# Performance work log

Measured on AMD Instinct MI355X. Metric: run time of the kernel, lower is better.

Reference implementation:

```python
import jax, jax.numpy as jnp
import numpy as np

NODES = 512
SCALE_S, SCALE_M, SCALE_L = 512, 1024, 2048
BATCH = 16
SEQ = SCALE_S + SCALE_M + SCALE_L
EPS = 1e-5


def setup_inputs() -> dict:
    key = jax.random.key(0)
    ks = jax.random.split(key, 10)
    sd = 1.0 / np.sqrt(NODES)
    inp = {
        "x": jax.random.normal(ks[0], (BATCH, SEQ, NODES), dtype=jnp.float32),
        "gamma": jnp.ones((NODES,), jnp.float32),
        "beta": jnp.zeros((NODES,), jnp.float32),
        "Wqkv_s": jax.random.normal(ks[1], (NODES, 3 * NODES), jnp.float32) * sd,
        "bqkv_s": jnp.zeros((3 * NODES,), jnp.float32),
        "Wqkv_m": jax.random.normal(ks[2], (NODES, 3 * NODES), jnp.float32) * sd,
        "bqkv_m": jnp.zeros((3 * NODES,), jnp.float32),
        "Wqkv_l": jax.random.normal(ks[3], (NODES, 3 * NODES), jnp.float32) * sd,
        "bqkv_l": jnp.zeros((3 * NODES,), jnp.float32),
        "Wout": jax.random.normal(ks[4], (NODES, NODES), jnp.float32) * sd,
        "bout": jnp.zeros((NODES,), jnp.float32),
    }
    return inp


def _attn_block(x, W, b, scaling):
    # x: [B, L, N]; fused QKV projection then single-head attention
    qkv = jnp.einsum("bln,nm->blm", x, W) + b
    q, k, v = jnp.split(qkv, 3, axis=-1)
    scores = jnp.einsum("bqn,bkn->bqk", q, k) * scaling
    attn = jax.nn.softmax(scores, axis=-1)
    return jnp.einsum("bqk,bkn->bqn", attn, v)


def reference(x, gamma, beta, Wqkv_s, bqkv_s, Wqkv_m, bqkv_m, Wqkv_l, bqkv_l, Wout, bout):
    res = x
    mu = jnp.mean(x, axis=-1, keepdims=True)
    var = jnp.mean(jnp.square(x - mu), axis=-1, keepdims=True)
    h = (x - mu) * jax.lax.rsqrt(var + EPS) * gamma + beta

    scaling = NODES ** (-0.5)
    xs = h[:, :SCALE_S, :]
    xm = h[:, SCALE_S:SCALE_S + SCALE_M, :]
    xl = h[:, SCALE_S + SCALE_M:SCALE_S + SCALE_M + SCALE_L, :]

    out_s = _attn_block(xs, Wqkv_s, bqkv_s, scaling)
    out_m = _attn_block(xm, Wqkv_m, bqkv_m, scaling)
    out_l = _attn_block(xl, Wqkv_l, bqkv_l, scaling)

    out = jnp.concatenate([out_s, out_m, out_l], axis=1)
    out = jnp.einsum("bln,nm->blm", out, Wout) + bout
    return out + res
```

## Files before the change

kernel.cpp:

```cpp
#include <hip/hip_runtime.h>
#include <stdint.h>

typedef __bf16 bf16;
typedef __bf16 bf16x8 __attribute__((ext_vector_type(8)));
typedef __bf16 bf16x4 __attribute__((ext_vector_type(4)));
typedef float f32x4 __attribute__((ext_vector_type(4)));

#define MFMA16(a, b, c) __builtin_amdgcn_mfma_f32_16x16x32_bf16(a, b, c, 0, 0, 0)

typedef const __attribute__((address_space(1))) uint32_t* gas_t;
typedef __attribute__((address_space(3))) uint32_t* las_t;

__device__ __forceinline__ void gload16(const void* g, void* l) {
  __builtin_amdgcn_global_load_lds((gas_t)g, (las_t)l, 16, 0, 0);
}

__device__ __forceinline__ void stage_tile(const bf16* __restrict__ A, int lda,
                                           const bf16* __restrict__ Bt, int ldb,
                                           int m0, int n0, int k0, bf16* Ad,
                                           bf16* Bd, int w, int r8, int cs) {
#pragma unroll
  for (int i = 0; i < 4; ++i) {
    const int ii = (w << 2) + i;
    const int row = (ii << 3) + r8;
    gload16(A + (size_t)(m0 + row) * lda + k0 + (cs << 3), Ad + (ii << 9));
    gload16(Bt + (size_t)(n0 + row) * ldb + k0 + (cs << 3), Bd + (ii << 9));
  }
}

__device__ __forceinline__ void compute_tile(const bf16* As, const bf16* Bs,
                                             f32x4 (*acc)[4], int lane, int wm,
                                             int wn) {
#pragma unroll
  for (int kk = 0; kk < 2; ++kk) {
    bf16x8 af[4], bfr[4];
#pragma unroll
    for (int mi = 0; mi < 4; ++mi) {
      const int r = wm * 64 + mi * 16 + (lane & 15);
      const int ch = kk * 4 + (lane >> 4);
      af[mi] = *(const bf16x8*)((const char*)As + r * 128 + ((ch ^ (r & 7)) << 4));
    }
#pragma unroll
    for (int ni = 0; ni < 4; ++ni) {
      const int r = wn * 64 + ni * 16 + (lane & 15);
      const int ch = kk * 4 + (lane >> 4);
      bfr[ni] = *(const bf16x8*)((const char*)Bs + r * 128 + ((ch ^ (r & 7)) << 4));
    }
#pragma unroll
    for (int mi = 0; mi < 4; ++mi)
#pragma unroll
      for (int ni = 0; ni < 4; ++ni)
        acc[mi][ni] = MFMA16(af[mi], bfr[ni], acc[mi][ni]);
  }
}

__device__ __forceinline__ void gemm_core(const bf16* __restrict__ A, int lda,
                                          const bf16* __restrict__ Bt, int ldb,
                                          int nk, int m0, int n0,
                                          bf16 (*smem)[128 * 64],
                                          f32x4 (*acc)[4]) {
  const int t = threadIdx.x;
  const int lane = t & 63, w = t >> 6;
  const int wm = w >> 1, wn = w & 1;
  const int r8 = lane >> 3;
  const int cs = (lane & 7) ^ r8;

  stage_tile(A, lda, Bt, ldb, m0, n0, 0, smem[0], smem[2], w, r8, cs);
  __syncthreads();
  int cur = 0;
  for (int kt = 0; kt < nk; ++kt) {
    if (kt + 1 < nk)
      stage_tile(A, lda, Bt, ldb, m0, n0, (kt + 1) << 6, smem[cur ^ 1],
                 smem[2 + (cur ^ 1)], w, r8, cs);
    compute_tile(smem[cur], smem[2 + cur], acc, lane, wm, wn);
    __syncthreads();
    cur ^= 1;
  }
}

__device__ __forceinline__ void epi_put(float* lds, const f32x4* accmi,
                                        int lane, int wm, int wn) {
#pragma unroll
  for (int ni = 0; ni < 4; ++ni) {
    const int c = wn * 64 + ni * 16 + (lane & 15);
    const int lr0 = wm * 16 + ((lane >> 4) << 2);
#pragma unroll
    for (int r = 0; r < 4; ++r) {
      const int lr = lr0 + r;
      lds[(lr << 7) + ((((c >> 2) ^ (lr & 7)) << 2) | (c & 3))] = accmi[ni][r];
    }
  }
}

__device__ __forceinline__ void epi_get(const float* lds, int t, f32x4* v) {
  const int lr = t >> 3, ch0 = (t & 7) << 2;
#pragma unroll
  for (int j = 0; j < 4; ++j)
    v[j] = *(const f32x4*)(lds + (lr << 7) + (((ch0 + j) ^ (lr & 7)) << 2));
}

__global__ __launch_bounds__(256) void transpose_all(
    const float* __restrict__ Ws, const float* __restrict__ Wm,
    const float* __restrict__ Wl, const float* __restrict__ Wo,
    bf16* __restrict__ os, bf16* __restrict__ om, bf16* __restrict__ ol,
    bf16* __restrict__ oo) {
  __shared__ float tile[32][33];
  const int id = blockIdx.x;
  const float* in;
  bf16* outp;
  int N, bx;
  if (id < 768) { in = Ws; outp = os; N = 1536; bx = id; }
  else if (id < 1536) { in = Wm; outp = om; N = 1536; bx = id - 768; }
  else if (id < 2304) { in = Wl; outp = ol; N = 1536; bx = id - 1536; }
  else { in = Wo; outp = oo; N = 512; bx = id - 2304; }
  const int nbx = N >> 5;
  const int n0 = (bx % nbx) * 32, k0 = (bx / nbx) * 32;
  const int tx = threadIdx.x, ty = threadIdx.y;
#pragma unroll
  for (int i = 0; i < 4; ++i)
    tile[ty * 4 + i][tx] = in[(size_t)(k0 + ty * 4 + i) * N + n0 + tx];
  __syncthreads();
#pragma unroll
  for (int i = 0; i < 4; ++i)
    outp[(size_t)(n0 + ty * 4 + i) * 512 + k0 + tx] = (bf16)tile[tx][ty * 4 + i];
}

__global__ __launch_bounds__(256) void conv_v(const float* __restrict__ Ws,
                                              const float* __restrict__ Wm,
                                              const float* __restrict__ Wl,
                                              bf16* __restrict__ Bs,
                                              bf16* __restrict__ Bm,
                                              bf16* __restrict__ Bl) {
  int id = blockIdx.x;
  const float* W;
  bf16* B;
  if (id < 256) { W = Ws; B = Bs; }
  else if (id < 512) { W = Wm; B = Bm; id -= 256; }
  else { W = Wl; B = Bl; id -= 512; }
  const int idx = (id * 256 + threadIdx.x) * 4;
  const int k = idx >> 9, j = idx & 511;
  float4 v = *(const float4*)(W + (size_t)k * 1536 + 1024 + j);
  bf16x4 o = {(bf16)v.x, (bf16)v.y, (bf16)v.z, (bf16)v.w};
  *(bf16x4*)(B + idx) = o;
}

__global__ __launch_bounds__(256) void wprep(const bf16* __restrict__ wto,
                                             const bf16* __restrict__ Bs,
                                             const bf16* __restrict__ Bm,
                                             const bf16* __restrict__ Bl,
                                             bf16* __restrict__ ws_,
                                             bf16* __restrict__ wm_,
                                             bf16* __restrict__ wl_) {
  __shared__ bf16 smem[4][128 * 64];
  const int t = threadIdx.x, lane = t & 63, w = t >> 6;
  const int wm = w >> 1, wn = w & 1;
  const int id = blockIdx.x;
  const int sc = id >> 4, rem = id & 15;
  const bf16* Bv;
  bf16* dst;
  if (sc == 0) { Bv = Bs; dst = ws_; }
  else if (sc == 1) { Bv = Bm; dst = wm_; }
  else { Bv = Bl; dst = wl_; }
  dst += 1024 * 512;
  const int m0 = (rem >> 2) << 7, n0 = (rem & 3) << 7;

  f32x4 acc[4][4];
#pragma unroll
  for (int i = 0; i < 4; ++i)
#pragma unroll
    for (int j = 0; j < 4; ++j) acc[i][j] = (f32x4)0.0f;

  gemm_core(wto, 512, Bv, 512, 8, m0, n0, smem, acc);

  float* et = (float*)smem;
#pragma unroll
  for (int mi = 0; mi < 4; ++mi) epi_put(et + (mi << 12), acc[mi], lane, wm, wn);
  __syncthreads();
  const int lr = t >> 3, c0l = (t & 7) << 4;
#pragma unroll
  for (int mi = 0; mi < 4; ++mi) {
    f32x4 v[4];
    epi_get(et + (mi << 12), t, v);
    const int grow = m0 + ((lr >> 4) << 6) + mi * 16 + (lr & 15);
    bf16x8 o0, o1;
#pragma unroll
    for (int j = 0; j < 4; ++j)
#pragma unroll
      for (int k = 0; k < 4; ++k) {
        const bf16 val = (bf16)v[j][k];
        if (j < 2) o0[j * 4 + k] = val;
        else o1[(j - 2) * 4 + k] = val;
      }
    bf16* d = dst + (size_t)grow * 512 + n0 + c0l;
    *(bf16x8*)d = o0;
    *(bf16x8*)(d + 8) = o1;
  }
}

__global__ __launch_bounds__(512) void bias_prep(const float* __restrict__ bs,
                                                 const float* __restrict__ bm,
                                                 const float* __restrict__ bl,
                                                 const float* __restrict__ Wout,
                                                 float* __restrict__ ps,
                                                 float* __restrict__ pm,
                                                 float* __restrict__ pl) {
  const float* b;
  float* p;
  if (blockIdx.x == 0) { b = bs; p = ps; }
  else if (blockIdx.x == 1) { b = bm; p = pm; }
  else { b = bl; p = pl; }
  const int t = threadIdx.x;
  p[t] = b[t];
  p[512 + t] = b[512 + t];
  float acc = 0.0f;
  for (int n = 0; n < 512; ++n) acc += b[1024 + n] * Wout[(size_t)n * 512 + t];
  p[1024 + t] = acc;
}

__global__ __launch_bounds__(256) void ln_kernel(const float* __restrict__ x,
                                                 const float* __restrict__ gamma,
                                                 const float* __restrict__ beta,
                                                 bf16* __restrict__ h) {
  const int t = threadIdx.x, lane = t & 63, w = t >> 6;
  const int row = blockIdx.x * 4 + w;
  const float* xr = x + (size_t)row * 512 + lane * 8;
  float4 v0 = *(const float4*)xr;
  float4 v1 = *(const float4*)(xr + 4);
  float s = v0.x + v0.y + v0.z + v0.w + v1.x + v1.y + v1.z + v1.w;
  float q = v0.x * v0.x + v0.y * v0.y + v0.z * v0.z + v0.w * v0.w +
            v1.x * v1.x + v1.y * v1.y + v1.z * v1.z + v1.w * v1.w;
#pragma unroll
  for (int off = 1; off < 64; off <<= 1) {
    s += __shfl_xor(s, off);
    q += __shfl_xor(q, off);
  }
  const float mean = s * (1.0f / 512.0f);
  const float var = q * (1.0f / 512.0f) - mean * mean;
  const float rs = rsqrtf(var + 1e-5f);
  float4 g0 = *(const float4*)(gamma + lane * 8);
  float4 g1 = *(const float4*)(gamma + lane * 8 + 4);
  float4 b0 = *(const float4*)(beta + lane * 8);
  float4 b1 = *(const float4*)(beta + lane * 8 + 4);
  const int bb = row / 3584;
  const int sp = row - bb * 3584;
  size_t drow;
  if (sp < 512)
    drow = (size_t)bb * 512 + sp;
  else if (sp < 1536)
    drow = 8192 + (size_t)bb * 1024 + (sp - 512);
  else
    drow = 24576 + (size_t)bb * 2048 + (sp - 1536);
  bf16x8 ov = {(bf16)((v0.x - mean) * rs * g0.x + b0.x),
               (bf16)((v0.y - mean) * rs * g0.y + b0.y),
               (bf16)((v0.z - mean) * rs * g0.z + b0.z),
               (bf16)((v0.w - mean) * rs * g0.w + b0.w),
               (bf16)((v1.x - mean) * rs * g1.x + b1.x),
               (bf16)((v1.y - mean) * rs * g1.y + b1.y),
               (bf16)((v1.z - mean) * rs * g1.z + b1.z),
               (bf16)((v1.w - mean) * rs * g1.w + b1.w)};
  *(bf16x8*)(h + drow * 512 + lane * 8) = ov;
}

__device__ __forceinline__ void qkv_body(const bf16* __restrict__ A,
                                         const bf16* __restrict__ Bt,
                                         const float* __restrict__ bias,
                                         bf16* __restrict__ qk,
                                         bf16* __restrict__ vt, int l2L,
                                         int lgs, bf16 (*smem)[128 * 64]) {
  const int t = threadIdx.x, lane = t & 63, w = t >> 6;
  const int wm = w >> 1, wn = w & 1;
  const int m0 = (lgs / 12) << 7;
  const int n0 = (lgs % 12) << 7;
  const int L = 1 << l2L;

  f32x4 acc[4][4];
#pragma unroll
  for (int i = 0; i < 4; ++i)
#pragma unroll
    for (int j = 0; j < 4; ++j) acc[i][j] = (f32x4)0.0f;

  gemm_core(A, 512, Bt, 512, 8, m0, n0, smem, acc);

  if (n0 < 1024) {
    float* et = (float*)smem;
#pragma unroll
    for (int mi = 0; mi < 4; ++mi) epi_put(et + (mi << 12), acc[mi], lane, wm, wn);
    __syncthreads();
    const int lr = t >> 3, c0l = (t & 7) << 4;
    const int gcol = n0 + c0l;
#pragma unroll
    for (int mi = 0; mi < 4; ++mi) {
      f32x4 v[4];
      epi_get(et + (mi << 12), t, v);
      const int grow = m0 + ((lr >> 4) << 6) + mi * 16 + (lr & 15);
      bf16x8 o0, o1;
#pragma unroll
      for (int j = 0; j < 4; ++j) {
        float4 bv = *(const float4*)(bias + gcol + j * 4);
#pragma unroll
        for (int k = 0; k < 4; ++k) {
          const bf16 val = (bf16)(v[j][k] + ((const float*)&bv)[k]);
          if (j < 2) o0[j * 4 + k] = val;
          else o1[(j - 2) * 4 + k] = val;
        }
      }
      bf16* dst = qk + (size_t)grow * 1024 + gcol;
      *(bf16x8*)dst = o0;
      *(bf16x8*)(dst + 8) = o1;
    }
  } else {
#pragma unroll
    for (int ni = 0; ni < 4; ++ni) {
      const int col = n0 + wn * 64 + ni * 16 + (lane & 15);
      const float bv = bias[col];
#pragma unroll
      for (int mi = 0; mi < 4; ++mi) {
        const int rb = m0 + wm * 64 + mi * 16 + ((lane >> 4) << 2);
        const int d = col - 1024;
        const int bi = rb >> l2L;
        const int kv = rb & (L - 1);
        bf16x4 pk = {(bf16)(acc[mi][ni][0] + bv), (bf16)(acc[mi][ni][1] + bv),
                     (bf16)(acc[mi][ni][2] + bv), (bf16)(acc[mi][ni][3] + bv)};
        *(bf16x4*)(vt + ((size_t)bi * 512 + d) * L + kv) = pk;
      }
    }
  }
}

__global__ __launch_bounds__(256) void qkv_all(
    const bf16* __restrict__ h, const bf16* __restrict__ wt_s,
    const bf16* __restrict__ wt_m, const bf16* __restrict__ wt_l,
    const float* __restrict__ pb_s, const float* __restrict__ pb_m,
    const float* __restrict__ pb_l, bf16* __restrict__ qk,
    bf16* __restrict__ vt) {
  __shared__ bf16 smem[4][128 * 64];
  const int lg = (blockIdx.x & 7) * (5376 >> 3) + (blockIdx.x >> 3);
  if (lg < 768) {
    qkv_body(h, wt_s, pb_s, qk, vt, 9, lg, smem);
  } else if (lg < 2304) {
    qkv_body(h + 8192ull * 512, wt_m, pb_m, qk + 8192ull * 1024,
             vt + 4194304ull, 10, lg - 768, smem);
  } else {
    qkv_body(h + 24576ull * 512, wt_l, pb_l, qk + 24576ull * 1024,
             vt + 12582912ull, 11, lg - 2304, smem);
  }
}

__global__ __launch_bounds__(256) void sgemm_one(const bf16* __restrict__ qkp,
                                                 bf16* __restrict__ Cb, int l2L,
                                                 int b0, float scl2, int nblk,
                                                 float* __restrict__ psum) {
  __shared__ bf16 smem[4][128 * 64];
  const int t = threadIdx.x, lane = t & 63, w = t >> 6;
  const int wm = w >> 1, wn = w & 1;
  const int L = 1 << l2L;
  const int l2nt = l2L - 7;
  const int lgs = (blockIdx.x & 7) * (nblk >> 3) + (blockIdx.x >> 3);
  const int bi = lgs >> (2 * l2nt);
  const int rem = lgs & ((1 << (2 * l2nt)) - 1);
  const int m0 = (rem >> l2nt) << 7;
  const int n0 = (rem & ((1 << l2nt) - 1)) << 7;

  const bf16* Ab = qkp + (size_t)(b0 + bi) * L * 1024;
  const bf16* Bb = Ab + 512;
  bf16* C = Cb + (size_t)bi * L * L;

  f32x4 acc[4][4];
#pragma unroll
  for (int i = 0; i < 4; ++i)
#pragma unroll
    for (int j = 0; j < 4; ++j) acc[i][j] = (f32x4)0.0f;

  gemm_core(Ab, 1024, Bb, 1024, 8, m0, n0, smem, acc);

  float* et = (float*)smem;
#pragma unroll
  for (int mi = 0; mi < 4; ++mi) epi_put(et + (mi << 12), acc[mi], lane, wm, wn);
  __syncthreads();
  const int lr = t >> 3, c0l = (t & 7) << 4;
  const int tilej = n0 >> 7;
#pragma unroll
  for (int mi = 0; mi < 4; ++mi) {
    f32x4 v[4];
    epi_get(et + (mi << 12), t, v);
    const int grow = m0 + ((lr >> 4) << 6) + mi * 16 + (lr & 15);
    bf16x8 o0, o1;
    float ps = 0.0f;
#pragma unroll
    for (int j = 0; j < 4; ++j)
#pragma unroll
      for (int k = 0; k < 4; ++k) {
        const float e = exp2f(v[j][k] * scl2);
        const bf16 val = (bf16)e;
        ps += (float)val;
        if (j < 2) o0[j * 4 + k] = val;
        else o1[(j - 2) * 4 + k] = val;
      }
    bf16* dst = C + (size_t)grow * L + n0 + c0l;
    *(bf16x8*)dst = o0;
    *(bf16x8*)(dst + 8) = o1;
    ps += __shfl_xor(ps, 1);
    ps += __shfl_xor(ps, 2);
    ps += __shfl_xor(ps, 4);
    if ((t & 7) == 0) psum[((size_t)(bi * L + grow) << 4) + tilej] = ps;
  }
}

__global__ __launch_bounds__(256) void pv_one(const bf16* __restrict__ sb,
                                              const bf16* __restrict__ vtp,
                                              float* __restrict__ out,
                                              const float* __restrict__ x,
                                              const float* __restrict__ bout,
                                              int l2L, int b0, int seqoff,
                                              int nblk,
                                              const float* __restrict__ psum) {
  __shared__ bf16 smem[4][128 * 64];
  const int t = threadIdx.x, lane = t & 63, w = t >> 6;
  const int wm = w >> 1, wn = w & 1;
  const int L = 1 << l2L;
  const int l2nt = l2L - 7;
  const int ntile = 1 << l2nt;
  const int lgs = (blockIdx.x & 7) * (nblk >> 3) + (blockIdx.x >> 3);
  const int bi = lgs >> (l2nt + 2);
  const int rem = lgs & ((1 << (l2nt + 2)) - 1);
  const int m0 = (rem >> 2) << 7;
  const int n0 = (rem & 3) << 7;
  const int b = b0 + bi;

  const bf16* Ab = sb + (size_t)bi * L * L;
  const bf16* Bb = vtp + (size_t)b * 512 * L;

  f32x4 acc[4][4];
#pragma unroll
  for (int i = 0; i < 4; ++i)
#pragma unroll
    for (int j = 0; j < 4; ++j) acc[i][j] = (f32x4)0.0f;

  gemm_core(Ab, L, Bb, L, L >> 6, m0, n0, smem, acc);

  float* et = (float*)smem;
#pragma unroll
  for (int mi = 0; mi < 4; ++mi) epi_put(et + (mi << 12), acc[mi], lane, wm, wn);
  __syncthreads();
  const int lr = t >> 3, c0l = (t & 7) << 4;
  const int gcol = n0 + c0l;
  float4 bvv[4];
#pragma unroll
  for (int j = 0; j < 4; ++j) bvv[j] = *(const float4*)(bout + gcol + j * 4);
#pragma unroll
  for (int mi = 0; mi < 4; ++mi) {
    f32x4 v[4];
    epi_get(et + (mi << 12), t, v);
    const int grow = m0 + ((lr >> 4) << 6) + mi * 16 + (lr & 15);
    const float* pr = psum + ((size_t)(bi * L + grow) << 4);
    float rs = 0.0f;
    for (int j = 0; j < ntile; ++j) rs += pr[j];
    const float inv = 1.0f / rs;
    const size_t g = (size_t)b * 3584 + seqoff + grow;
    const float* xs = x + g * 512 + gcol;
    float* os = out + g * 512 + gcol;
#pragma unroll
    for (int j = 0; j < 4; ++j) {
      float4 xv = *(const float4*)(xs + j * 4);
      float4 ov;
      ov.x = v[j][0] * inv + bvv[j].x + xv.x;
      ov.y = v[j][1] * inv + bvv[j].y + xv.y;
      ov.z = v[j][2] * inv + bvv[j].z + xv.z;
      ov.w = v[j][3] * inv + bvv[j].w + xv.w;
      *(float4*)(os + j * 4) = ov;
    }
  }
}

extern "C" void kernel_launch(void* const* d_in, const int* in_sizes, int n_in,
                              void* d_out, int out_size, void* d_ws,
                              size_t ws_size, hipStream_t stream) {
  const float* x = (const float*)d_in[0];
  const float* gamma = (const float*)d_in[1];
  const float* beta = (const float*)d_in[2];
  const float* Wq_s = (const float*)d_in[3];
  const float* bq_s = (const float*)d_in[4];
  const float* Wq_m = (const float*)d_in[5];
  const float* bq_m = (const float*)d_in[6];
  const float* Wq_l = (const float*)d_in[7];
  const float* bq_l = (const float*)d_in[8];
  const float* Wout = (const float*)d_in[9];
  const float* bout = (const float*)d_in[10];
  float* out = (float*)d_out;

  char* ws = (char*)d_ws;
  bf16* h = (bf16*)(ws);
  bf16* qk = (bf16*)(ws + 58720256ull);
  bf16* vt = (bf16*)(ws + 176160768ull);
  bf16* wt_s = (bf16*)(ws + 234881024ull);
  bf16* wt_m = (bf16*)(ws + 236453888ull);
  bf16* wt_l = (bf16*)(ws + 238026752ull);
  bf16* wt_o = (bf16*)(ws + 239599616ull);
  float* psum = (float*)(ws + 240123904ull);

  char* od = (char*)d_out;
  bf16* Bv_s = (bf16*)(od + 110000128ull);
  bf16* Bv_m = Bv_s + 262144;
  bf16* Bv_l = Bv_m + 262144;
  float* pb_s = (float*)(od + 111573504ull);
  float* pb_m = pb_s + 1536;
  float* pb_l = pb_m + 1536;

  transpose_all<<<2560, dim3(32, 8), 0, stream>>>(Wq_s, Wq_m, Wq_l, Wout, wt_s,
                                                  wt_m, wt_l, wt_o);
  conv_v<<<768, 256, 0, stream>>>(Wq_s, Wq_m, Wq_l, Bv_s, Bv_m, Bv_l);
  wprep<<<48, 256, 0, stream>>>(wt_o, Bv_s, Bv_m, Bv_l, wt_s, wt_m, wt_l);
  bias_prep<<<3, 512, 0, stream>>>(bq_s, bq_m, bq_l, Wout, pb_s, pb_m, pb_l);

  ln_kernel<<<14336, 256, 0, stream>>>(x, gamma, beta, h);

  qkv_all<<<5376, 256, 0, stream>>>(h, wt_s, wt_m, wt_l, pb_s, pb_m, pb_l, qk,
                                    vt);

  const float scale = 0.04419417382415922f;
  const float scl2 = scale * 1.44269504088896f;
  bf16* P = h;

  sgemm_one<<<256, 256, 0, stream>>>(qk, P, 9, 0, scl2, 256, psum);
  pv_one<<<256, 256, 0, stream>>>(P, vt, out, x, bout, 9, 0, 0, 256, psum);

  sgemm_one<<<1024, 256, 0, stream>>>(qk + 8192ull * 1024, P, 10, 0, scl2,
                                      1024, psum);
  pv_one<<<512, 256, 0, stream>>>(P, vt + 4194304ull, out, x, bout, 10, 0, 512,
                                  512, psum);

  for (int q = 0; q < 4; ++q) {
    sgemm_one<<<1024, 256, 0, stream>>>(qk + 24576ull * 1024, P, 11, q * 4,
                                        scl2, 1024, psum);
    pv_one<<<256, 256, 0, stream>>>(P, vt + 12582912ull, out, x, bout, 11,
                                    q * 4, 1536, 256, psum);
  }
}
```

Before: 639.1 us.

## Merge small/medium scale attention launches and double large-scale batch chunk

```diff
diff --git a/kernel.cpp b/kernel.cpp
--- a/kernel.cpp
+++ b/kernel.cpp
@@ -346,16 +346,15 @@
   }
 }
 
-__global__ __launch_bounds__(256) void sgemm_one(const bf16* __restrict__ qkp,
-                                                 bf16* __restrict__ Cb, int l2L,
-                                                 int b0, float scl2, int nblk,
-                                                 float* __restrict__ psum) {
-  __shared__ bf16 smem[4][128 * 64];
+__device__ __forceinline__ void sgemm_body(const bf16* __restrict__ qkp,
+                                           bf16* __restrict__ Cb, int l2L,
+                                           int b0, int lgs, float scl2,
+                                           float* __restrict__ psum, int psb,
+                                           bf16 (*smem)[128 * 64]) {
   const int t = threadIdx.x, lane = t & 63, w = t >> 6;
   const int wm = w >> 1, wn = w & 1;
   const int L = 1 << l2L;
   const int l2nt = l2L - 7;
-  const int lgs = (blockIdx.x & 7) * (nblk >> 3) + (blockIdx.x >> 3);
   const int bi = lgs >> (2 * l2nt);
   const int rem = lgs & ((1 << (2 * l2nt)) - 1);
   const int m0 = (rem >> l2nt) << 7;
@@ -402,8 +401,109 @@
     ps += __shfl_xor(ps, 1);
     ps += __shfl_xor(ps, 2);
     ps += __shfl_xor(ps, 4);
-    if ((t & 7) == 0) psum[((size_t)(bi * L + grow) << 4) + tilej] = ps;
-  }
+    if ((t & 7) == 0) psum[((size_t)(psb + bi * L + grow) << 4) + tilej] = ps;
+  }
+}
+
+__global__ __launch_bounds__(256) void sgemm_sm(const bf16* __restrict__ qk,
+                                                bf16* __restrict__ PS,
+                                                bf16* __restrict__ PM,
+                                                float scl2,
+                                                float* __restrict__ psum) {
+  __shared__ bf16 smem[4][128 * 64];
+  const int lg = (blockIdx.x & 7) * (1280 >> 3) + (blockIdx.x >> 3);
+  if (lg < 256)
+    sgemm_body(qk, PS, 9, 0, lg, scl2, psum, 0, smem);
+  else
+    sgemm_body(qk + 8192ull * 1024, PM, 10, 0, lg - 256, scl2, psum, 8192,
+               smem);
+}
+
+__global__ __launch_bounds__(256) void sgemm_one(const bf16* __restrict__ qkp,
+                                                 bf16* __restrict__ Cb, int l2L,
+                                                 int b0, float scl2, int nblk,
+                                                 float* __restrict__ psum) {
+  __shared__ bf16 smem[4][128 * 64];
+  const int lg = (blockIdx.x & 7) * (nblk >> 3) + (blockIdx.x >> 3);
+  sgemm_body(qkp, Cb, l2L, b0, lg, scl2, psum, 0, smem);
+}
+
+__device__ __forceinline__ void pv_body(const bf16* __restrict__ sb,
+                                        const bf16* __restrict__ vtp,
+                                        float* __restrict__ out,
+                                        const float* __restrict__ x,
+                                        const float* __restrict__ bout, int l2L,
+                                        int b0, int seqoff, int lgs,
+                                        const float* __restrict__ psum, int psb,
+                                        bf16 (*smem)[128 * 64]) {
+  const int t = threadIdx.x, lane = t & 63, w = t >> 6;
+  const int wm = w >> 1, wn = w & 1;
+  const int L = 1 << l2L;
+  const int l2nt = l2L - 7;
+  const int ntile = 1 << l2nt;
+  const int bi = lgs >> (l2nt + 2);
+  const int rem = lgs & ((1 << (l2nt + 2)) - 1);
+  const int m0 = (rem >> 2) << 7;
+  const int n0 = (rem & 3) << 7;
+  const int b = b0 + bi;
+
+  const bf16* Ab = sb + (size_t)bi * L * L;
+  const bf16* Bb = vtp + (size_t)b * 512 * L;
+
+  f32x4 acc[4][4];
+#pragma unroll
+  for (int i = 0; i < 4; ++i)
+#pragma unroll
+    for (int j = 0; j < 4; ++j) acc[i][j] = (f32x4)0.0f;
+
+  gemm_core(Ab, L, Bb, L, L >> 6, m0, n0, smem, acc);
+
+  float* et = (float*)smem;
+#pragma unroll
+  for (int mi = 0; mi < 4; ++mi) epi_put(et + (mi << 12), acc[mi], lane, wm, wn);
+  __syncthreads();
+  const int lr = t >> 3, c0l = (t & 7) << 4;
+  const int gcol = n0 + c0l;
+  float4 bvv[4];
+#pragma unroll
+  for (int j = 0; j < 4; ++j) bvv[j] = *(const float4*)(bout + gcol + j * 4);
+#pragma unroll
+  for (int mi = 0; mi < 4; ++mi) {
+    f32x4 v[4];
+    epi_get(et + (mi << 12), t, v);
+    const int grow = m0 + ((lr >> 4) << 6) + mi * 16 + (lr & 15);
+    const float* pr = psum + ((size_t)(psb + bi * L + grow) << 4);
+    float rs = 0.0f;
+    for (int j = 0; j < ntile; ++j) rs += pr[j];
+    const float inv = 1.0f / rs;
+    const size_t g = (size_t)b * 3584 + seqoff + grow;
+    const float* xs = x + g * 512 + gcol;
+    float* os = out + g * 512 + gcol;
+#pragma unroll
+    for (int j = 0; j < 4; ++j) {
+      float4 xv = *(const float4*)(xs + j * 4);
+      float4 ov;
+      ov.x = v[j][0] * inv + bvv[j].x + xv.x;
+      ov.y = v[j][1] * inv + bvv[j].y + xv.y;
+      ov.z = v[j][2] * inv + bvv[j].z + xv.z;
+      ov.w = v[j][3] * inv + bvv[j].w + xv.w;
+      *(float4*)(os + j * 4) = ov;
+    }
+  }
+}
+
+__global__ __launch_bounds__(256) void pv_sm(
+    const bf16* __restrict__ PS, const bf16* __restrict__ PM,
+    const bf16* __restrict__ vt, float* __restrict__ out,
+    const float* __restrict__ x, const float* __restrict__ bout,
+    const float* __restrict__ psum) {
+  __shared__ bf16 smem[4][128 * 64];
+  const int lg = (blockIdx.x & 7) * (768 >> 3) + (blockIdx.x >> 3);
+  if (lg < 256)
+    pv_body(PS, vt, out, x, bout, 9, 0, 0, lg, psum, 0, smem);
+  else
+    pv_body(PM, vt + 4194304ull, out, x, bout, 10, 0, 512, lg - 256, psum,
+            8192, smem);
 }
 
 __global__ __launch_bounds__(256) void pv_one(const bf16* __restrict__ sb,
@@ -415,61 +515,8 @@
                                               int nblk,
                                               const float* __restrict__ psum) {
   __shared__ bf16 smem[4][128 * 64];
-  const int t = threadIdx.x, lane = t & 63, w = t >> 6;
-  const int wm = w >> 1, wn = w & 1;
-  const int L = 1 << l2L;
-  const int l2nt = l2L - 7;
-  const int ntile = 1 << l2nt;
-  const int lgs = (blockIdx.x & 7) * (nblk >> 3) + (blockIdx.x >> 3);
-  const int bi = lgs >> (l2nt + 2);
-  const int rem = lgs & ((1 << (l2nt + 2)) - 1);
-  const int m0 = (rem >> 2) << 7;
-  const int n0 = (rem & 3) << 7;
-  const int b = b0 + bi;
-
-  const bf16* Ab = sb + (size_t)bi * L * L;
-  const bf16* Bb = vtp + (size_t)b * 512 * L;
-
-  f32x4 acc[4][4];
-#pragma unroll
-  for (int i = 0; i < 4; ++i)
-#pragma unroll
-    for (int j = 0; j < 4; ++j) acc[i][j] = (f32x4)0.0f;
-
-  gemm_core(Ab, L, Bb, L, L >> 6, m0, n0, smem, acc);
-
-  float* et = (float*)smem;
-#pragma unroll
-  for (int mi = 0; mi < 4; ++mi) epi_put(et + (mi << 12), acc[mi], lane, wm, wn);
-  __syncthreads();
-  const int lr = t >> 3, c0l = (t & 7) << 4;
-  const int gcol = n0 + c0l;
-  float4 bvv[4];
-#pragma unroll
-  for (int j = 0; j < 4; ++j) bvv[j] = *(const float4*)(bout + gcol + j * 4);
-#pragma unroll
-  for (int mi = 0; mi < 4; ++mi) {
-    f32x4 v[4];
-    epi_get(et + (mi << 12), t, v);
-    const int grow = m0 + ((lr >> 4) << 6) + mi * 16 + (lr & 15);
-    const float* pr = psum + ((size_t)(bi * L + grow) << 4);
-    float rs = 0.0f;
-    for (int j = 0; j < ntile; ++j) rs += pr[j];
-    const float inv = 1.0f / rs;
-    const size_t g = (size_t)b * 3584 + seqoff + grow;
-    const float* xs = x + g * 512 + gcol;
-    float* os = out + g * 512 + gcol;
-#pragma unroll
-    for (int j = 0; j < 4; ++j) {
-      float4 xv = *(const float4*)(xs + j * 4);
-      float4 ov;
-      ov.x = v[j][0] * inv + bvv[j].x + xv.x;
-      ov.y = v[j][1] * inv + bvv[j].y + xv.y;
-      ov.z = v[j][2] * inv + bvv[j].z + xv.z;
-      ov.w = v[j][3] * inv + bvv[j].w + xv.w;
-      *(float4*)(os + j * 4) = ov;
-    }
-  }
+  const int lg = (blockIdx.x & 7) * (nblk >> 3) + (blockIdx.x >> 3);
+  pv_body(sb, vtp, out, x, bout, l2L, b0, seqoff, lg, psum, 0, smem);
 }
 
 extern "C" void kernel_launch(void* const* d_in, const int* in_sizes, int n_in,
@@ -519,20 +566,18 @@
 
   const float scale = 0.04419417382415922f;
   const float scl2 = scale * 1.44269504088896f;
-  bf16* P = h;
-
-  sgemm_one<<<256, 256, 0, stream>>>(qk, P, 9, 0, scl2, 256, psum);
-  pv_one<<<256, 256, 0, stream>>>(P, vt, out, x, bout, 9, 0, 0, 256, psum);
-
-  sgemm_one<<<1024, 256, 0, stream>>>(qk + 8192ull * 1024, P, 10, 0, scl2,
-                                      1024, psum);
-  pv_one<<<512, 256, 0, stream>>>(P, vt + 4194304ull, out, x, bout, 10, 0, 512,
-                                  512, psum);
-
-  for (int q = 0; q < 4; ++q) {
-    sgemm_one<<<1024, 256, 0, stream>>>(qk + 24576ull * 1024, P, 11, q * 4,
-                                        scl2, 1024, psum);
-    pv_one<<<256, 256, 0, stream>>>(P, vt + 12582912ull, out, x, bout, 11,
-                                    q * 4, 1536, 256, psum);
-  }
-}
+
+  bf16* PS = h;
+  bf16* PM = h + 4194304ull;
+
+  sgemm_sm<<<1280, 256, 0, stream>>>(qk, PS, PM, scl2, psum);
+  pv_sm<<<768, 256, 0, stream>>>(PS, PM, vt, out, x, bout, psum);
+
+  bf16* PL = h;
+  for (int b0 = 0; b0 < 16; b0 += 8) {
+    sgemm_one<<<2048, 256, 0, stream>>>(qk + 24576ull * 1024, PL, 11, b0, scl2,
+                                        2048, psum);
+    pv_one<<<512, 256, 0, stream>>>(PL, vt + 12582912ull, out, x, bout, 11, b0,
+                                    1536, 512, psum);
+  }
+}
```

New measurement: 544.0 us. 1.17x faster.
